# Performance work log

Hardware: AMD Instinct MI355X
Metric: run time of the kernel (lower is better)

## Reference

```python
import jax, jax.numpy as jnp
import numpy as np

C, N, D, B = 1000, 128, 512, 4096


def setup_inputs() -> dict:
    key = jax.random.key(0)
    k1, k2, k3, k4, k5 = jax.random.split(key, 5)
    return {
        "memory": jax.random.normal(k1, (C, N, D), dtype=jnp.float32),
        "confidences": jax.random.uniform(k2, (C, N), dtype=jnp.float32),
        "batch_features": jax.random.normal(k3, (B, D), dtype=jnp.float32),
        "batch_targets": jax.random.normal(k4, (B, C), dtype=jnp.float32),
        "batch_confidences": jax.random.randint(k5, (B,), 0, 1000, dtype=jnp.int64),
        "selected_mask": jnp.arange(B, dtype=jnp.int64),
    }


def reference(memory, confidences, batch_features, batch_targets,
              batch_confidences, selected_mask):
    # Gather selected samples (selected_mask is an index tensor in the original).
    feats = batch_features[selected_mask]                      # [S, D]
    tgts = jnp.argmax(batch_targets[selected_mask], axis=1)    # [S] class indices
    confs = batch_confidences[selected_mask].astype(memory.dtype)  # [S] (.long() cast -> int values)

    def step(carry, x):
        mem, cf = carry                       # mem: [C,N,D], cf: [C,N]
        f, c, conf = x                        # f: [D], c: scalar int, conf: scalar float
        row = mem[c]                          # [N, D]
        rcf = cf[c]                           # [N]
        cond = conf > rcf[-1]
        # Faithful to original: memory row 0 is dropped, feature appended at end;
        # confidences are NOT shifted, only last slot is overwritten.
        shifted = jnp.concatenate([row[1:], f[None, :]], axis=0)  # [N, D]
        ncf = rcf.at[-1].set(conf)
        order = jnp.argsort(-ncf)             # stable descending sort of confidences
        new_row = shifted[order]
        new_cf = ncf[order]
        mem = mem.at[c].set(jnp.where(cond, new_row, row))
        cf = cf.at[c].set(jnp.where(cond, new_cf, rcf))
        return (mem, cf), None

    (mem, cf), _ = jax.lax.scan(step, (memory, confidences), (feats, tgts, confs))
    return mem
```

## Files before the change

### kernel.cpp

```cpp
#include <hip/hip_runtime.h>

#define C_CLASSES 1000
#define N_SLOTS   128
#define D_DIM     512
#define B_SAMPLES 4096

__global__ __launch_bounds__(256) void argmax_kernel(
    const float* __restrict__ targets,
    const int*   __restrict__ mask,
    int*         __restrict__ cls)
{
    const int wave = threadIdx.x >> 6;
    const int lane = threadIdx.x & 63;
    const int p = blockIdx.x * 4 + wave;
    if (p >= B_SAMPLES) return;

    const int sample = mask[p];
    const float* row = targets + (long long)sample * C_CLASSES;

    float bestv = -INFINITY;
    int   besti = 0;
    for (int k = lane; k < C_CLASSES; k += 64) {
        float v = row[k];
        if (v > bestv) { bestv = v; besti = k; }
    }
    for (int off = 32; off > 0; off >>= 1) {
        float ov = __shfl_down(bestv, off, 64);
        int   oi = __shfl_down(besti, off, 64);
        if (ov > bestv || (ov == bestv && oi < besti)) { bestv = ov; besti = oi; }
    }
    if (lane == 0) cls[p] = besti;
}

__global__ __launch_bounds__(64) void simulate_kernel(
    const float* __restrict__ confidences,
    const int*   __restrict__ bconf,
    const int*   __restrict__ mask,
    const int*   __restrict__ cls,
    int*         __restrict__ src_out)
{
    const int c    = blockIdx.x;
    const int lane = threadIdx.x;

    __shared__ float cf[N_SLOTS];
    __shared__ int   src[N_SLOTS];
    __shared__ float ncf[N_SLOTS];
    __shared__ int   nsrc[N_SLOTS];

    cf[lane]      = confidences[c * N_SLOTS + lane];
    cf[lane + 64] = confidences[c * N_SLOTS + lane + 64];
    src[lane]      = lane;
    src[lane + 64] = lane + 64;
    __syncthreads();

    for (int base = 0; base < B_SAMPLES; base += 64) {
        const int p     = base + lane;
        const int myc   = cls[p];
        const int mys   = mask[p];
        const int mycnf = bconf[mys];

        unsigned long long m = __ballot(myc == c);
        while (m) {
            const int b = __ffsll(m) - 1;
            m &= m - 1;

            const float conf = (float)__shfl(mycnf, b, 64);
            const int   feat = __shfl(mys, b, 64);
            const float last = cf[N_SLOTS - 1];

            if (conf > last) {
                ncf[lane]  = cf[lane];
                nsrc[lane] = src[lane + 1];
                if (lane + 64 < N_SLOTS - 1) {
                    ncf[lane + 64]  = cf[lane + 64];
                    nsrc[lane + 64] = src[lane + 65];
                } else {
                    ncf[N_SLOTS - 1]  = conf;
                    nsrc[N_SLOTS - 1] = -(feat + 1);
                }
                __syncthreads();

                const float v0 = ncf[lane], v1 = ncf[lane + 64];
                int r0 = 0, r1 = 0;
                for (int j = 0; j < N_SLOTS; ++j) {
                    const float vj = ncf[j];
                    r0 += (vj > v0) || (vj == v0 && j < lane);
                    r1 += (vj > v1) || (vj == v1 && j < lane + 64);
                }
                const int s0 = nsrc[lane], s1 = nsrc[lane + 64];
                __syncthreads();
                cf[r0] = v0;  src[r0] = s0;
                cf[r1] = v1;  src[r1] = s1;
                __syncthreads();
            }
        }
    }

    src_out[c * N_SLOTS + lane]      = src[lane];
    src_out[c * N_SLOTS + lane + 64] = src[lane + 64];
}

__global__ __launch_bounds__(256) void writeback_kernel(
    const float* __restrict__ memory,
    const float* __restrict__ feats,
    const int*   __restrict__ src,
    float*       __restrict__ out)
{
    const int wave = threadIdx.x >> 6;
    const int lane = threadIdx.x & 63;
    const long long row = (long long)blockIdx.x * 4 + wave;
    const int c = (int)(row >> 7);
    const int s = src[row];

    const float* sp;
    if (s >= 0) sp = memory + ((long long)c * N_SLOTS + s) * D_DIM;
    else        sp = feats + (long long)(-(s + 1)) * D_DIM;
    float* dp = out + row * D_DIM;

    const float4* sp4 = (const float4*)sp;
    float4* dp4 = (float4*)dp;
    float4 a = sp4[lane];
    float4 b = sp4[lane + 64];
    dp4[lane]      = a;
    dp4[lane + 64] = b;
}

extern "C" void kernel_launch(void* const* d_in, const int* in_sizes, int n_in,
                              void* d_out, int out_size, void* d_ws, size_t ws_size,
                              hipStream_t stream) {
    const float* memory  = (const float*)d_in[0];
    const float* confid  = (const float*)d_in[1];
    const float* feats   = (const float*)d_in[2];
    const float* targets = (const float*)d_in[3];
    const int*   bconf   = (const int*)d_in[4];
    const int*   mask    = (const int*)d_in[5];
    float* out = (float*)d_out;

    int* cls = (int*)d_ws;
    int* src = cls + B_SAMPLES;

    argmax_kernel<<<(B_SAMPLES + 3) / 4, 256, 0, stream>>>(targets, mask, cls);
    simulate_kernel<<<C_CLASSES, 64, 0, stream>>>(confid, bconf, mask, cls, src);
    writeback_kernel<<<(C_CLASSES * N_SLOTS) / 4, 256, 0, stream>>>(memory, feats, src, out);
}
```

Baseline: 525.9 us.

## Fuse simulation with writeback, compact per-class sample list, vectorize argmax loads

Merges the per-class slot simulation and the row-copy writeback into one 512-thread block per class, which removes the intermediate src buffer and one kernel launch. Each block first stages the class ids in shared memory and builds a compacted list of samples for its class with ballot and popcount. The simulation then walks only those samples instead of scanning all 4096 with a ballot loop. Rows are copied with nontemporal vector loads and stores, and the argmax kernel now reads float4 vectors. The risk is that the serial simulation runs in larger blocks with block-wide barriers, and only 1000 blocks do the whole 262MB copy, which could limit memory parallelism.

```diff
diff --git a/kernel.cpp b/kernel.cpp
--- a/kernel.cpp
+++ b/kernel.cpp
@@ -4,6 +4,8 @@
 #define N_SLOTS   128
 #define D_DIM     512
 #define B_SAMPLES 4096
+
+typedef float v4f __attribute__((ext_vector_type(4)));
 
 __global__ __launch_bounds__(256) void argmax_kernel(
     const float* __restrict__ targets,
@@ -16,13 +18,21 @@
     if (p >= B_SAMPLES) return;
 
     const int sample = mask[p];
-    const float* row = targets + (long long)sample * C_CLASSES;
+    const v4f* row4 = (const v4f*)(targets + (long long)sample * C_CLASSES);
 
     float bestv = -INFINITY;
     int   besti = 0;
-    for (int k = lane; k < C_CLASSES; k += 64) {
-        float v = row[k];
-        if (v > bestv) { bestv = v; besti = k; }
+    #pragma unroll
+    for (int t = 0; t < 4; ++t) {
+        const int k4 = lane + t * 64;
+        if (k4 < C_CLASSES / 4) {
+            v4f v4 = row4[k4];
+            #pragma unroll
+            for (int cc = 0; cc < 4; ++cc) {
+                float v = v4[cc];
+                if (v > bestv) { bestv = v; besti = k4 * 4 + cc; }
+            }
+        }
     }
     for (int off = 32; off > 0; off >>= 1) {
         float ov = __shfl_down(bestv, off, 64);
@@ -32,97 +42,105 @@
     if (lane == 0) cls[p] = besti;
 }
 
-__global__ __launch_bounds__(64) void simulate_kernel(
+__global__ __launch_bounds__(512) void sim_write_kernel(
+    const float* __restrict__ memory,
     const float* __restrict__ confidences,
+    const float* __restrict__ feats,
     const int*   __restrict__ bconf,
     const int*   __restrict__ mask,
     const int*   __restrict__ cls,
-    int*         __restrict__ src_out)
+    float*       __restrict__ out)
 {
     const int c    = blockIdx.x;
-    const int lane = threadIdx.x;
+    const int tid  = threadIdx.x;
+    const int lane = tid & 63;
+    const int wave = tid >> 6;
 
-    __shared__ float cf[N_SLOTS];
-    __shared__ int   src[N_SLOTS];
-    __shared__ float ncf[N_SLOTS];
-    __shared__ int   nsrc[N_SLOTS];
+    __shared__ int   s_cls[B_SAMPLES];
+    __shared__ int   s_plist[B_SAMPLES];
+    __shared__ float s_cf[N_SLOTS];
+    __shared__ int   s_src[N_SLOTS];
+    __shared__ float s_ncf[N_SLOTS];
+    __shared__ int   s_nsrc[N_SLOTS];
+    __shared__ float s_conf[N_SLOTS];
+    __shared__ int   s_feat[N_SLOTS];
+    __shared__ int   s_K;
 
-    cf[lane]      = confidences[c * N_SLOTS + lane];
-    cf[lane + 64] = confidences[c * N_SLOTS + lane + 64];
-    src[lane]      = lane;
-    src[lane + 64] = lane + 64;
+    for (int i = tid; i < B_SAMPLES; i += 512) s_cls[i] = cls[i];
+    if (tid < N_SLOTS) {
+        s_cf[tid]  = confidences[c * N_SLOTS + tid];
+        s_src[tid] = tid;
+    }
     __syncthreads();
 
-    for (int base = 0; base < B_SAMPLES; base += 64) {
-        const int p     = base + lane;
-        const int myc   = cls[p];
-        const int mys   = mask[p];
-        const int mycnf = bconf[mys];
+    if (wave == 0) {
+        int k = 0;
+        for (int i = 0; i < B_SAMPLES / 64; ++i) {
+            const int p  = i * 64 + lane;
+            const int cv = s_cls[p];
+            const unsigned long long m = __ballot(cv == c);
+            if (cv == c) {
+                const int r = __popcll(m & ((1ull << lane) - 1ull));
+                s_plist[k + r] = p;
+            }
+            k += __popcll(m);
+        }
+        if (lane == 0) s_K = k;
+    }
+    __syncthreads();
+    const int K = s_K;
 
-        unsigned long long m = __ballot(myc == c);
-        while (m) {
-            const int b = __ffsll(m) - 1;
-            m &= m - 1;
+    for (int base = 0; base < K; base += N_SLOTS) {
+        const int chunk = min(N_SLOTS, K - base);
+        if (tid < chunk) {
+            const int p   = s_plist[base + tid];
+            const int mys = mask[p];
+            s_feat[tid] = mys;
+            s_conf[tid] = (float)bconf[mys];
+        }
+        __syncthreads();
 
-            const float conf = (float)__shfl(mycnf, b, 64);
-            const int   feat = __shfl(mys, b, 64);
-            const float last = cf[N_SLOTS - 1];
+        for (int k = 0; k < chunk; ++k) {
+            const float conf = s_conf[k];
+            const int   feat = s_feat[k];
+            const float last = s_cf[N_SLOTS - 1];
 
             if (conf > last) {
-                ncf[lane]  = cf[lane];
-                nsrc[lane] = src[lane + 1];
-                if (lane + 64 < N_SLOTS - 1) {
-                    ncf[lane + 64]  = cf[lane + 64];
-                    nsrc[lane + 64] = src[lane + 65];
-                } else {
-                    ncf[N_SLOTS - 1]  = conf;
-                    nsrc[N_SLOTS - 1] = -(feat + 1);
+                if (tid < N_SLOTS) {
+                    s_ncf[tid]  = (tid == N_SLOTS - 1) ? conf : s_cf[tid];
+                    s_nsrc[tid] = (tid == N_SLOTS - 1) ? -(feat + 1)
+                                                       : s_src[tid + 1];
                 }
                 __syncthreads();
 
-                const float v0 = ncf[lane], v1 = ncf[lane + 64];
-                int r0 = 0, r1 = 0;
-                for (int j = 0; j < N_SLOTS; ++j) {
-                    const float vj = ncf[j];
-                    r0 += (vj > v0) || (vj == v0 && j < lane);
-                    r1 += (vj > v1) || (vj == v1 && j < lane + 64);
+                float v = 0.f; int sv = 0; int r = 0;
+                if (tid < N_SLOTS) {
+                    v = s_ncf[tid]; sv = s_nsrc[tid];
+                    for (int j = 0; j < N_SLOTS; ++j) {
+                        const float vj = s_ncf[j];
+                        r += (vj > v) || (vj == v && j < tid);
+                    }
                 }
-                const int s0 = nsrc[lane], s1 = nsrc[lane + 64];
                 __syncthreads();
-                cf[r0] = v0;  src[r0] = s0;
-                cf[r1] = v1;  src[r1] = s1;
+                if (tid < N_SLOTS) { s_cf[r] = v; s_src[r] = sv; }
                 __syncthreads();
             }
         }
+        __syncthreads();
     }
 
-    src_out[c * N_SLOTS + lane]      = src[lane];
-    src_out[c * N_SLOTS + lane + 64] = src[lane + 64];
-}
-
-__global__ __launch_bounds__(256) void writeback_kernel(
-    const float* __restrict__ memory,
-    const float* __restrict__ feats,
-    const int*   __restrict__ src,
-    float*       __restrict__ out)
-{
-    const int wave = threadIdx.x >> 6;
-    const int lane = threadIdx.x & 63;
-    const long long row = (long long)blockIdx.x * 4 + wave;
-    const int c = (int)(row >> 7);
-    const int s = src[row];
-
-    const float* sp;
-    if (s >= 0) sp = memory + ((long long)c * N_SLOTS + s) * D_DIM;
-    else        sp = feats + (long long)(-(s + 1)) * D_DIM;
-    float* dp = out + row * D_DIM;
-
-    const float4* sp4 = (const float4*)sp;
-    float4* dp4 = (float4*)dp;
-    float4 a = sp4[lane];
-    float4 b = sp4[lane + 64];
-    dp4[lane]      = a;
-    dp4[lane + 64] = b;
+    #pragma unroll 4
+    for (int r = wave; r < N_SLOTS; r += 8) {
+        const int s = s_src[r];
+        const v4f* sp = (s >= 0)
+            ? (const v4f*)(memory + ((long long)c * N_SLOTS + s) * D_DIM)
+            : (const v4f*)(feats + (long long)(-(s + 1)) * D_DIM);
+        v4f* dp = (v4f*)(out + ((long long)c * N_SLOTS + r) * D_DIM);
+        v4f a = __builtin_nontemporal_load(sp + lane);
+        v4f b = __builtin_nontemporal_load(sp + lane + 64);
+        __builtin_nontemporal_store(a, dp + lane);
+        __builtin_nontemporal_store(b, dp + lane + 64);
+    }
 }
 
 extern "C" void kernel_launch(void* const* d_in, const int* in_sizes, int n_in,
@@ -137,9 +155,8 @@
     float* out = (float*)d_out;
 
     int* cls = (int*)d_ws;
-    int* src = cls + B_SAMPLES;
 
     argmax_kernel<<<(B_SAMPLES + 3) / 4, 256, 0, stream>>>(targets, mask, cls);
-    simulate_kernel<<<C_CLASSES, 64, 0, stream>>>(confid, bconf, mask, cls, src);
-    writeback_kernel<<<(C_CLASSES * N_SLOTS) / 4, 256, 0, stream>>>(memory, feats, src, out);
+    sim_write_kernel<<<C_CLASSES, 512, 0, stream>>>(
+        memory, confid, feats, bconf, mask, cls, out);
 }
```

Result: faster. 456.2 us (-13.2%).
